# Kernel tuning notes

Hardware: AMD Instinct MI355X
Metric: run time of the kernel (lower is better)

Reference implementation:

```python
import jax, jax.numpy as jnp
import numpy as np


def _shift(x, n):
    # torch.roll along the last (angular) axis
    return jnp.roll(x, n, axis=3)


def _flip(x, n):
    # mirror about index n along the last axis: out[..., i] = x[..., (n - i) mod W]
    return jnp.roll(jnp.flip(x, axis=3), n + 1, axis=3)


def setup_inputs() -> dict:
    key = jax.random.key(0)
    k1, k2, k3 = jax.random.split(key, 3)
    B, C, H, W = 16, 96, 96, 96
    x = jax.random.normal(k1, (B, C, H, W), dtype=jnp.float32)
    s = jax.random.normal(k2, (B, 5), dtype=jnp.float32)
    w = jax.random.uniform(k3, (B, C, H, W), dtype=jnp.float32) + 0.1  # keep denominator well-conditioned
    return {"x": x, "s": s, "w": w}


def reference(x, s, w):
    # s.shape[1] == 5 branch of SymmetryControl (square symmetry: 3 rotations + 2 mirrors)
    sg = jax.nn.sigmoid(s).reshape(s.shape[0], -1, 1, 1)  # [B,5,1,1]
    step = x.shape[3] // 8

    x90 = _shift(x, step * 2)
    x180 = _shift(x, step * 4)
    x270 = _shift(x, step * 6)
    x90f = _flip(x, step * 2 - 1)
    x180f = _flip(x, step * 4 - 1)

    w90 = sg[:, 0:1] * _shift(w, step * 2)
    w180 = sg[:, 1:2] * _shift(w, step * 4)
    w270 = sg[:, 2:3] * _shift(w, step * 6)
    w90f = sg[:, 3:4] * _flip(w, step * 2 - 1)
    w180f = sg[:, 4:5] * _flip(w, step * 4 - 1)

    a = (w * x + w90 * x90 + w180 * x180 + w270 * x270
         + w90f * x90f + w180f * x180f)
    b = w + w90 + w180 + w270 + w90f + w180f
    return a / b
```

## Files before the change

kernel.cpp:

```cpp
#include <hip/hip_runtime.h>


#define WDIM 96
#define RPB  9216
#define QPB  (RPB / 2)
#define WPB  4
#define GRID 2048

__device__ __forceinline__ float bperm(int byteidx, float v) {
    return __int_as_float(__builtin_amdgcn_ds_bpermute(byteidx, __float_as_int(v)));
}

__global__ __launch_bounds__(64 * WPB)
void symctl_kernel(const float* __restrict__ x,
                   const float* __restrict__ s,
                   const float* __restrict__ w,
                   float* __restrict__ out,
                   int total_q) {
    const int lane = threadIdx.x & 63;
    const int tl   = lane & 31;
    const int hsel = lane & 32;
    const int h    = lane >> 5;

    const int gw = blockIdx.x * WPB + (threadIdx.x >> 6);
    const int nw = gridDim.x * WPB;

    const int span = (total_q + nw - 1) / nw;
    const int q0 = gw * span;
    const int q1 = min(q0 + span, total_q);
    if (q0 >= q1) return;

    const int i90  = (hsel | ((tl -  8) & 31)) << 2;
    const int i180 = (hsel | ((tl - 16) & 31)) << 2;
    const int i270 = (hsel | ((tl +  8) & 31)) << 2;
    const int f90  = (hsel | (( 7 - tl) & 31)) << 2;
    const int f180 = (hsel | ((15 - tl) & 31)) << 2;

    int bcur = -1;
    float sg0 = 0.f, sg1 = 0.f, sg2 = 0.f, sg3 = 0.f, sg4 = 0.f;

    size_t off = (size_t)(2 * q0 + h) * WDIM + 3 * tl;
    float3 xv = *(const float3*)(x + off);
    float3 wv = *(const float3*)(w + off);

    for (int q = q0; q < q1; ++q) {
        const float3 xc = xv;
        const float3 wc = wv;

        if (q + 1 < q1) {
            const size_t noff = (size_t)(2 * (q + 1) + h) * WDIM + 3 * tl;
            xv = *(const float3*)(x + noff);
            wv = *(const float3*)(w + noff);
        }

        const int b = q / QPB;
        if (b != bcur) {
            bcur = b;
            const float* sb = s + b * 5;
            sg0 = 1.0f / (1.0f + __expf(-sb[0]));
            sg1 = 1.0f / (1.0f + __expf(-sb[1]));
            sg2 = 1.0f / (1.0f + __expf(-sb[2]));
            sg3 = 1.0f / (1.0f + __expf(-sb[3]));
            sg4 = 1.0f / (1.0f + __expf(-sb[4]));
        }

        const float p0 = xc.x * wc.x;
        const float p1 = xc.y * wc.y;
        const float p2 = xc.z * wc.z;

        float n0 = p0,   n1 = p1,   n2 = p2;
        float d0 = wc.x, d1 = wc.y, d2 = wc.z;

        n0 = fmaf(sg0, bperm(i90,  p0),   n0);
        n1 = fmaf(sg0, bperm(i90,  p1),   n1);
        n2 = fmaf(sg0, bperm(i90,  p2),   n2);
        d0 = fmaf(sg0, bperm(i90,  wc.x), d0);
        d1 = fmaf(sg0, bperm(i90,  wc.y), d1);
        d2 = fmaf(sg0, bperm(i90,  wc.z), d2);

        n0 = fmaf(sg1, bperm(i180, p0),   n0);
        n1 = fmaf(sg1, bperm(i180, p1),   n1);
        n2 = fmaf(sg1, bperm(i180, p2),   n2);
        d0 = fmaf(sg1, bperm(i180, wc.x), d0);
        d1 = fmaf(sg1, bperm(i180, wc.y), d1);
        d2 = fmaf(sg1, bperm(i180, wc.z), d2);

        n0 = fmaf(sg2, bperm(i270, p0),   n0);
        n1 = fmaf(sg2, bperm(i270, p1),   n1);
        n2 = fmaf(sg2, bperm(i270, p2),   n2);
        d0 = fmaf(sg2, bperm(i270, wc.x), d0);
        d1 = fmaf(sg2, bperm(i270, wc.y), d1);
        d2 = fmaf(sg2, bperm(i270, wc.z), d2);

        n0 = fmaf(sg3, bperm(f90,  p2),   n0);
        n1 = fmaf(sg3, bperm(f90,  p1),   n1);
        n2 = fmaf(sg3, bperm(f90,  p0),   n2);
        d0 = fmaf(sg3, bperm(f90,  wc.z), d0);
        d1 = fmaf(sg3, bperm(f90,  wc.y), d1);
        d2 = fmaf(sg3, bperm(f90,  wc.x), d2);

        n0 = fmaf(sg4, bperm(f180, p2),   n0);
        n1 = fmaf(sg4, bperm(f180, p1),   n1);
        n2 = fmaf(sg4, bperm(f180, p0),   n2);
        d0 = fmaf(sg4, bperm(f180, wc.z), d0);
        d1 = fmaf(sg4, bperm(f180, wc.y), d1);
        d2 = fmaf(sg4, bperm(f180, wc.x), d2);

        float3 o;
        o.x = n0 * __builtin_amdgcn_rcpf(d0);
        o.y = n1 * __builtin_amdgcn_rcpf(d1);
        o.z = n2 * __builtin_amdgcn_rcpf(d2);
        *(float3*)(out + (size_t)(2 * q + h) * WDIM + 3 * tl) = o;
    }
}

extern "C" void kernel_launch(void* const* d_in, const int* in_sizes, int n_in,
                              void* d_out, int out_size, void* d_ws, size_t ws_size,
                              hipStream_t stream) {
    const float* x = (const float*)d_in[0];
    const float* s = (const float*)d_in[1];
    const float* w = (const float*)d_in[2];
    float* out = (float*)d_out;

    const int n_rows  = in_sizes[0] / WDIM;
    const int total_q = n_rows / 2;

    const int waves_needed = total_q;
    int grid = GRID;
    if (grid * WPB > waves_needed) grid = (waves_needed + WPB - 1) / WPB;

    dim3 block(64 * WPB);
    symctl_kernel<<<grid, block, 0, stream>>>(x, s, w, out, total_q);
}
```

Baseline: 158.7 us.

## Replace persistent strided loop with fixed 8-row-per-wave grid and batched loads

Replaces the persistent grid-stride loop, which processed one row pair per iteration with a one-deep prefetch, with a non-persistent launch. Each wave now handles exactly 8 rows and issues all of its x and w loads up front before computing. The batch index and sigmoids are computed once per block, which removes the per-iteration division and branch. The launch grows to many more blocks to raise memory-level parallelism, and the code assumes rows divide evenly into waves and blocks and that a block never spans a batch boundary.

```diff
diff --git a/kernel.cpp b/kernel.cpp
--- a/kernel.cpp
+++ b/kernel.cpp
@@ -3,9 +3,8 @@
 
 #define WDIM 96
 #define RPB  9216
-#define QPB  (RPB / 2)
 #define WPB  4
-#define GRID 2048
+#define RPW  8
 
 __device__ __forceinline__ float bperm(int byteidx, float v) {
     return __int_as_float(__builtin_amdgcn_ds_bpermute(byteidx, __float_as_int(v)));
@@ -15,20 +14,30 @@
 void symctl_kernel(const float* __restrict__ x,
                    const float* __restrict__ s,
                    const float* __restrict__ w,
-                   float* __restrict__ out,
-                   int total_q) {
+                   float* __restrict__ out) {
     const int lane = threadIdx.x & 63;
     const int tl   = lane & 31;
     const int hsel = lane & 32;
     const int h    = lane >> 5;
 
-    const int gw = blockIdx.x * WPB + (threadIdx.x >> 6);
-    const int nw = gridDim.x * WPB;
+    const int wid = blockIdx.x * WPB + (threadIdx.x >> 6);
+    const int base = (RPW * wid + h) * WDIM + 3 * tl;
 
-    const int span = (total_q + nw - 1) / nw;
-    const int q0 = gw * span;
-    const int q1 = min(q0 + span, total_q);
-    if (q0 >= q1) return;
+    float3 xa[4], wa[4];
+#pragma unroll
+    for (int k = 0; k < 4; ++k)
+        xa[k] = *(const float3*)(x + base + k * (2 * WDIM));
+#pragma unroll
+    for (int k = 0; k < 4; ++k)
+        wa[k] = *(const float3*)(w + base + k * (2 * WDIM));
+
+    const int b = (blockIdx.x * (RPW * WPB)) / RPB;
+    const float* sb = s + b * 5;
+    const float sg0 = 1.0f / (1.0f + __expf(-sb[0]));
+    const float sg1 = 1.0f / (1.0f + __expf(-sb[1]));
+    const float sg2 = 1.0f / (1.0f + __expf(-sb[2]));
+    const float sg3 = 1.0f / (1.0f + __expf(-sb[3]));
+    const float sg4 = 1.0f / (1.0f + __expf(-sb[4]));
 
     const int i90  = (hsel | ((tl -  8) & 31)) << 2;
     const int i180 = (hsel | ((tl - 16) & 31)) << 2;
@@ -36,33 +45,10 @@
     const int f90  = (hsel | (( 7 - tl) & 31)) << 2;
     const int f180 = (hsel | ((15 - tl) & 31)) << 2;
 
-    int bcur = -1;
-    float sg0 = 0.f, sg1 = 0.f, sg2 = 0.f, sg3 = 0.f, sg4 = 0.f;
-
-    size_t off = (size_t)(2 * q0 + h) * WDIM + 3 * tl;
-    float3 xv = *(const float3*)(x + off);
-    float3 wv = *(const float3*)(w + off);
-
-    for (int q = q0; q < q1; ++q) {
-        const float3 xc = xv;
-        const float3 wc = wv;
-
-        if (q + 1 < q1) {
-            const size_t noff = (size_t)(2 * (q + 1) + h) * WDIM + 3 * tl;
-            xv = *(const float3*)(x + noff);
-            wv = *(const float3*)(w + noff);
-        }
-
-        const int b = q / QPB;
-        if (b != bcur) {
-            bcur = b;
-            const float* sb = s + b * 5;
-            sg0 = 1.0f / (1.0f + __expf(-sb[0]));
-            sg1 = 1.0f / (1.0f + __expf(-sb[1]));
-            sg2 = 1.0f / (1.0f + __expf(-sb[2]));
-            sg3 = 1.0f / (1.0f + __expf(-sb[3]));
-            sg4 = 1.0f / (1.0f + __expf(-sb[4]));
-        }
+#pragma unroll
+    for (int k = 0; k < 4; ++k) {
+        const float3 xc = xa[k];
+        const float3 wc = wa[k];
 
         const float p0 = xc.x * wc.x;
         const float p1 = xc.y * wc.y;
@@ -110,7 +96,7 @@
         o.x = n0 * __builtin_amdgcn_rcpf(d0);
         o.y = n1 * __builtin_amdgcn_rcpf(d1);
         o.z = n2 * __builtin_amdgcn_rcpf(d2);
-        *(float3*)(out + (size_t)(2 * q + h) * WDIM + 3 * tl) = o;
+        *(float3*)(out + base + k * (2 * WDIM)) = o;
     }
 }
 
@@ -122,13 +108,10 @@
     const float* w = (const float*)d_in[2];
     float* out = (float*)d_out;
 
-    const int n_rows  = in_sizes[0] / WDIM;
-    const int total_q = n_rows / 2;
-
-    const int waves_needed = total_q;
-    int grid = GRID;
-    if (grid * WPB > waves_needed) grid = (waves_needed + WPB - 1) / WPB;
+    const int n_rows = in_sizes[0] / WDIM;
+    const int waves  = n_rows / RPW;
+    const int grid   = waves / WPB;
 
     dim3 block(64 * WPB);
-    symctl_kernel<<<grid, block, 0, stream>>>(x, s, w, out, total_q);
+    symctl_kernel<<<grid, block, 0, stream>>>(x, s, w, out);
 }
```

After: 153.3 us. -3.4%, faster.
